# Performance work log

Measured on AMD Instinct MI355X. Metric: run time of the kernel, lower is better.

## Reference

```python
import jax, jax.numpy as jnp
import numpy as np

B, T, C, H = 2, 2048, 1024, 16
HD = C // H  # head dim = 64


def setup_inputs() -> dict:
    key = jax.random.key(0)
    ks = jax.random.split(key, 5)
    s = 1.0 / np.sqrt(C)
    return {
        "x": jax.random.normal(ks[0], (B, T, C), dtype=jnp.float32),
        "W_attn": jax.random.normal(ks[1], (3 * C, C), dtype=jnp.float32) * s,
        "b_attn": jax.random.normal(ks[2], (3 * C,), dtype=jnp.float32) * 0.02,
        "W_proj": jax.random.normal(ks[3], (C, C), dtype=jnp.float32) * s,
        "b_proj": jax.random.normal(ks[4], (C,), dtype=jnp.float32) * 0.02,
    }


def reference(x, W_attn, b_attn, W_proj, b_proj):
    Bx, Tx, Cx = x.shape
    # fused QKV projection (torch Linear: x @ W.T + b)
    qkv = x @ W_attn.T + b_attn                      # [B,T,3C]
    q, k, v = jnp.split(qkv, 3, axis=-1)
    # [B,T,C] -> [B,H,T,hd]
    q = q.reshape(Bx, Tx, H, HD).transpose(0, 2, 1, 3)
    k = k.reshape(Bx, Tx, H, HD).transpose(0, 2, 1, 3)
    v = v.reshape(Bx, Tx, H, HD).transpose(0, 2, 1, 3)
    scale = 1.0 / np.sqrt(HD)
    att = jnp.einsum('bhqd,bhkd->bhqk', q, k) * scale  # [B,H,T,T]
    causal = jnp.tril(jnp.ones((Tx, Tx), dtype=bool))
    att = jnp.where(causal[None, None], att, -jnp.inf)
    att = jax.nn.softmax(att, axis=-1)
    y = jnp.einsum('bhqk,bhkd->bhqd', att, v)          # [B,H,T,hd]
    y = y.transpose(0, 2, 1, 3).reshape(Bx, Tx, Cx)
    return y @ W_proj.T + b_proj
```

## Files before the change

### kernel.cpp

```cpp
#include <hip/hip_runtime.h>

typedef unsigned short ushort_t;
typedef __bf16 bf16x8 __attribute__((ext_vector_type(8)));
typedef float f32x4 __attribute__((ext_vector_type(4)));
typedef unsigned u32x4 __attribute__((ext_vector_type(4)));

__device__ inline ushort_t f2bf(float f) {
  unsigned int u = __builtin_bit_cast(unsigned int, f);
  u += 0x7fff + ((u >> 16) & 1);
  return (ushort_t)(u >> 16);
}

__device__ inline unsigned pk_bf(float a, float b) {
  unsigned r;
  asm("v_cvt_pk_bf16_f32 %0, %1, %2" : "=v"(r) : "v"(a), "v"(b));
  return r;
}

__device__ inline void async_ld16(const ushort_t* g, const ushort_t* l) {
  __builtin_amdgcn_global_load_lds(
      (const __attribute__((address_space(1))) void*)g,
      (__attribute__((address_space(3))) void*)l, 16, 0, 0);
}

template <int IMM>
__device__ inline void waitcnt_barrier() {
  asm volatile("" ::: "memory");
  __builtin_amdgcn_s_waitcnt(IMM);
  __builtin_amdgcn_s_barrier();
  asm volatile("" ::: "memory");
}

__global__ void cvt_all(const float* __restrict__ x, const float* __restrict__ wa,
                        const float* __restrict__ wp, ushort_t* __restrict__ xb,
                        ushort_t* __restrict__ wab, ushort_t* __restrict__ wpb) {
  int i = blockIdx.x * 256 + threadIdx.x;
  const float* src;
  ushort_t* dst;
  int off;
  if (i < 1048576) { src = x; dst = xb; off = i; }
  else if (i < 1835008) { src = wa; dst = wab; off = i - 1048576; }
  else { src = wp; dst = wpb; off = i - 1835008; }
  float4 f = ((const float4*)src)[off];
  unsigned long long p = (unsigned long long)f2bf(f.x)
      | ((unsigned long long)f2bf(f.y) << 16)
      | ((unsigned long long)f2bf(f.z) << 32)
      | ((unsigned long long)f2bf(f.w) << 48);
  ((unsigned long long*)dst)[off] = p;
}

template <int BM, int BN, int IM, int JN, int MODE, int TPB>
__global__ __launch_bounds__(TPB) void gemm_bt(
    const ushort_t* __restrict__ A, const ushort_t* __restrict__ B,
    const float* __restrict__ bias, float* __restrict__ Cf,
    ushort_t* __restrict__ Cb, ushort_t* __restrict__ vtb,
    int M, int N, int K, int ldc, float qscale) {
  constexpr int NWN = BN / (JN * 16);
  constexpr int NL = (BM + BN) * 32 / (TPB * 8);
  constexpr int WIMM = 0x0F70 | NL;
  __shared__ __align__(16) ushort_t As[3][BM * 32];
  __shared__ __align__(16) ushort_t Bs[3][BN * 32];
  const int tid = threadIdx.x;
  const int wave = tid >> 6, lane = tid & 63;
  const int quad = lane >> 4, l16 = lane & 15;
  const int wr = wave / NWN, wc = wave % NWN;
  const int wm = wr * IM * 16, wn = wc * JN * 16;
  const int m0 = blockIdx.y * BM, n0 = blockIdx.x * BN;
  const ushort_t* Ag = A + (size_t)m0 * K;
  const ushort_t* Bg = B + (size_t)n0 * K;
  const int slot = (quad ^ ((l16 >> 1) & 3)) * 8;
  f32x4 acc[IM][JN] = {};

  auto stage = [&](int kt, int bsel) {
    int k0 = kt * 32;
#pragma unroll
    for (int p = 0; p < BM * 4 / TPB; ++p) {
      int ci = p * TPB + tid;
      int row = ci >> 2, ch = (ci & 3) ^ ((ci >> 3) & 3);
      async_ld16(Ag + (size_t)row * K + k0 + ch * 8, As[bsel] + (p * TPB + wave * 64) * 8);
    }
#pragma unroll
    for (int p = 0; p < BN * 4 / TPB; ++p) {
      int ci = p * TPB + tid;
      int row = ci >> 2, ch = (ci & 3) ^ ((ci >> 3) & 3);
      async_ld16(Bg + (size_t)row * K + k0 + ch * 8, Bs[bsel] + (p * TPB + wave * 64) * 8);
    }
  };

  const int KT = K / 32;
  stage(0, 0);
  stage(1, 1);
  for (int kt = 0; kt < KT; ++kt) {
    waitcnt_barrier<WIMM>();
    if (kt + 2 < KT) stage(kt + 2, (kt + 2) % 3);
    const ushort_t* Ac = As[kt % 3];
    const ushort_t* Bc = Bs[kt % 3];
    bf16x8 af[IM], bfr[JN];
#pragma unroll
    for (int i = 0; i < IM; ++i)
      af[i] = *(const bf16x8*)(Ac + (wm + i * 16 + l16) * 32 + slot);
#pragma unroll
    for (int j = 0; j < JN; ++j)
      bfr[j] = *(const bf16x8*)(Bc + (wn + j * 16 + l16) * 32 + slot);
#pragma unroll
    for (int i = 0; i < IM; ++i)
#pragma unroll
      for (int j = 0; j < JN; ++j)
        acc[i][j] = __builtin_amdgcn_mfma_f32_16x16x32_bf16(af[i], bfr[j], acc[i][j], 0, 0, 0);
  }

  if (MODE == 1 && n0 >= 2048) {
#pragma unroll
    for (int j = 0; j < JN; ++j) {
      int col = n0 + wn + j * 16 + l16;
      int cv = col - 2048;
      float bv = bias[col];
      size_t rowbase = ((size_t)(cv >> 6)) * 64 + (cv & 63);
#pragma unroll
      for (int i = 0; i < IM; ++i) {
        int rowb = m0 + wm + i * 16 + quad * 4;
        int bb = rowb >> 11, t = rowb & 2047;
        uint2 pp;
        pp.x = pk_bf(acc[i][j][0] + bv, acc[i][j][1] + bv);
        pp.y = pk_bf(acc[i][j][2] + bv, acc[i][j][3] + bv);
        *(uint2*)(vtb + (((size_t)bb * 1024 + rowbase) * 2048 + t)) = pp;
      }
    }
    return;
  }
#pragma unroll
  for (int j = 0; j < JN; ++j) {
    int col = n0 + wn + j * 16 + l16;
    float bv = bias[col];
    float sc = (MODE == 1 && col < 1024) ? qscale : 1.0f;
#pragma unroll
    for (int i = 0; i < IM; ++i)
#pragma unroll
      for (int r = 0; r < 4; ++r) {
        int row = m0 + wm + i * 16 + quad * 4 + r;
        float v = (acc[i][j][r] + bv) * sc;
        if (MODE == 1)
          Cb[(size_t)row * ldc + col] = f2bf(v);
        else
          Cf[(size_t)row * ldc + col] = v;
      }
  }
}

__global__ __launch_bounds__(512, 4) void flash9(
    const ushort_t* __restrict__ qk, const ushort_t* __restrict__ vt,
    ushort_t* __restrict__ y) {
  __shared__ __align__(16) ushort_t Kb[2][2][4096];
  __shared__ __align__(16) ushort_t Vb[2][2][4096];
  const int tid = threadIdx.x, wave = tid >> 6, lane = tid & 63;
  const int quad = lane >> 4, l16 = lane & 15;
  const int r7 = l16 & 7;
  const int fK = (l16 & 3) | (((l16 >> 2) & 1) << 2);
  const int kbase = (16 * (l16 >> 2) + (l16 & 3)) * 64;
  const int xx = blockIdx.x, bh = blockIdx.y;
  const int Q = (bh < 16) ? (15 - xx) : xx;
  const int b = bh >> 4, h = bh & 15;
  const int bT = b * 2048;
  const int qw = Q * 128 + wave * 16;

  bf16x8 qf[2];
  {
    const ushort_t* qrow = qk + (size_t)(bT + qw + l16) * 2048 + h * 64 + quad * 8;
    qf[0] = *(const bf16x8*)(qrow);
    qf[1] = *(const bf16x8*)(qrow + 32);
  }

  auto stage1 = [&](int kt, int bsel, int u) {
    int k0 = kt * 64;
    int row = tid >> 3;
    int chk = (tid & 7) ^ ((row & 3) | (((row >> 4) & 1) << 2));
    int chv = (tid & 7) ^ (row & 7);
    async_ld16(qk + (size_t)(bT + k0 + row) * 2048 + 1024 + h * 64 + chk * 8,
               Kb[bsel][u] + wave * 512);
    async_ld16(vt + (size_t)(bh * 64 + row) * 2048 + k0 + chv * 8,
               Vb[bsel][u] + wave * 512);
  };
  auto stageS = [&](int s, int bsel) { stage1(2 * s, bsel, 0); stage1(2 * s + 1, bsel, 1); };

  f32x4 o[4] = {};
  float lac0 = 0.f, lac1 = 0.f;
  const int NS = Q + 1;

  stageS(0, 0);
  for (int s = 0; s < NS; ++s) {
    const int cur = s & 1;
    waitcnt_barrier<0x0F70>();
    if (s + 1 < NS) stageS(s + 1, cur ^ 1);
    __builtin_amdgcn_s_setprio(1);
    bf16x8 pf[2][2];
#pragma unroll
    for (int u = 0; u < 2; ++u) {
      const ushort_t* Kc = Kb[cur][u];
      const ushort_t* Vc = Vb[cur][u];
      bf16x8 kf[4][2];
#pragma unroll
      for (int j = 0; j < 4; ++j)
#pragma unroll
        for (int ks = 0; ks < 2; ++ks)
          kf[j][ks] = *(const bf16x8*)(Kc + kbase + j * 256 + (((ks * 4 + quad) ^ fK) * 8));
      f32x4 sr[4] = {};
#pragma unroll
      for (int ks = 0; ks < 2; ++ks)
#pragma unroll
        for (int j = 0; j < 4; ++j)
          sr[j] = __builtin_amdgcn_mfma_f32_16x16x32_bf16(kf[j][ks], qf[ks], sr[j], 0, 0, 0);
      if (s == NS - 1) {
        int qloc = qw + l16;
        int kt0 = (2 * s + u) * 64;
#pragma unroll
        for (int j = 0; j < 4; ++j)
#pragma unroll
          for (int r = 0; r < 4; ++r)
            if (kt0 + quad * 16 + j * 4 + r > qloc) sr[j][r] = -1e30f;
      }
#pragma unroll
      for (int j = 0; j < 4; ++j)
#pragma unroll
        for (int r = 0; r < 4; ++r)
          sr[j][r] = exp2f(sr[j][r]);
#pragma unroll
      for (int ks = 0; ks < 2; ++ks) {
        u32x4 w;
        w[0] = pk_bf(sr[2 * ks][0], sr[2 * ks][1]);
        w[1] = pk_bf(sr[2 * ks][2], sr[2 * ks][3]);
        w[2] = pk_bf(sr[2 * ks + 1][0], sr[2 * ks + 1][1]);
        w[3] = pk_bf(sr[2 * ks + 1][2], sr[2 * ks + 1][3]);
        pf[u][ks] = __builtin_bit_cast(bf16x8, w);
      }
#pragma unroll
      for (int j = 0; j < 4; ++j)
#pragma unroll
        for (int r = 0; r < 4; ++r) {
          if (j & 1) lac1 += sr[j][r]; else lac0 += sr[j][r];
        }
#pragma unroll
      for (int ks = 0; ks < 2; ++ks)
#pragma unroll
        for (int j = 0; j < 4; ++j) {
          bf16x8 vf = *(const bf16x8*)(Vc + (j * 16 + l16) * 64 + (((ks + 2 * quad) ^ r7) * 8));
          o[j] = __builtin_amdgcn_mfma_f32_16x16x32_bf16(vf, pf[u][ks], o[j], 0, 0, 0);
        }
    }
    __builtin_amdgcn_s_setprio(0);
  }

  {
    float l = lac0 + lac1;
    l += __shfl_xor(l, 16, 64);
    l += __shfl_xor(l, 32, 64);
    float inv = 1.f / l;
    size_t row = (size_t)(bT + qw + l16);
#pragma unroll
    for (int j = 0; j < 4; ++j) {
      uint2 pp;
      pp.x = pk_bf(o[j][0] * inv, o[j][1] * inv);
      pp.y = pk_bf(o[j][2] * inv, o[j][3] * inv);
      *(uint2*)(y + row * 1024 + h * 64 + j * 16 + quad * 4) = pp;
    }
  }
}

extern "C" void kernel_launch(void* const* d_in, const int* in_sizes, int n_in,
                              void* d_out, int out_size, void* d_ws, size_t ws_size,
                              hipStream_t stream) {
  const float* x  = (const float*)d_in[0];
  const float* Wa = (const float*)d_in[1];
  const float* ba = (const float*)d_in[2];
  const float* Wp = (const float*)d_in[3];
  const float* bp = (const float*)d_in[4];
  float* out = (float*)d_out;
  char* ws = (char*)d_ws;
  ushort_t* xb  = (ushort_t*)(ws);
  ushort_t* Wab = (ushort_t*)(ws + 8388608);
  ushort_t* Wpb = (ushort_t*)(ws + 14680064);
  ushort_t* qkb = (ushort_t*)(ws + 16777216);
  ushort_t* yb  = (ushort_t*)(ws + 33554432);
  ushort_t* vtb = (ushort_t*)(ws + 41943040);

  cvt_all<<<8192, 256, 0, stream>>>(x, Wa, Wp, xb, Wab, Wpb);
  gemm_bt<128, 128, 4, 2, 1, 512><<<dim3(24, 32), 512, 0, stream>>>(
      xb, Wab, ba, nullptr, qkb, vtb, 4096, 3072, 1024, 2048, 0.18033688011112042f);
  flash9<<<dim3(16, 32), 512, 0, stream>>>(qkb, vtb, yb);
  gemm_bt<64, 64, 2, 2, 0, 256><<<dim3(16, 64), 256, 0, stream>>>(
      yb, Wpb, bp, out, nullptr, nullptr, 4096, 1024, 1024, 1024, 1.0f);
}
```

Before: 178.4 us.

## Split long causal query tiles across two blocks with atomic-counter partial merge

Work in the flash attention kernel is rebalanced so that every block processes about the same number of key tiles. The long causal rows (query tiles 8-15) are split at key tile 17 between two blocks, and odd blocks also take a short query tile. The partial unnormalised outputs and row sums go to a float workspace, and an atomic counter per tile lets the second finisher combine both halves and write the result. The counters are reset in the conversion kernel. Occupancy hint drops from 4 to 2 blocks per CU, and the change adds extra global traffic and fences for the partials.

```diff
diff --git a/kernel.cpp b/kernel.cpp
--- a/kernel.cpp
+++ b/kernel.cpp
@@ -33,7 +33,9 @@
 
 __global__ void cvt_all(const float* __restrict__ x, const float* __restrict__ wa,
                         const float* __restrict__ wp, ushort_t* __restrict__ xb,
-                        ushort_t* __restrict__ wab, ushort_t* __restrict__ wpb) {
+                        ushort_t* __restrict__ wab, ushort_t* __restrict__ wpb,
+                        int* __restrict__ cnt) {
+  if (blockIdx.x == 0) cnt[threadIdx.x] = 0;
   int i = blockIdx.x * 256 + threadIdx.x;
   const float* src;
   ushort_t* dst;
@@ -147,31 +149,25 @@
   }
 }
 
-__global__ __launch_bounds__(512, 4) void flash9(
+__global__ __launch_bounds__(512, 2) void flash10(
     const ushort_t* __restrict__ qk, const ushort_t* __restrict__ vt,
-    ushort_t* __restrict__ y) {
+    ushort_t* __restrict__ y, float* __restrict__ pO, float* __restrict__ pl,
+    int* __restrict__ cnt) {
   __shared__ __align__(16) ushort_t Kb[2][2][4096];
   __shared__ __align__(16) ushort_t Vb[2][2][4096];
+  __shared__ int sflag;
   const int tid = threadIdx.x, wave = tid >> 6, lane = tid & 63;
   const int quad = lane >> 4, l16 = lane & 15;
   const int r7 = l16 & 7;
   const int fK = (l16 & 3) | (((l16 >> 2) & 1) << 2);
   const int kbase = (16 * (l16 >> 2) + (l16 & 3)) * 64;
-  const int xx = blockIdx.x, bh = blockIdx.y;
-  const int Q = (bh < 16) ? (15 - xx) : xx;
+  const int w = blockIdx.x, bh = blockIdx.y;
   const int b = bh >> 4, h = bh & 15;
   const int bT = b * 2048;
-  const int qw = Q * 128 + wave * 16;
-
-  bf16x8 qf[2];
-  {
-    const ushort_t* qrow = qk + (size_t)(bT + qw + l16) * 2048 + h * 64 + quad * 8;
-    qf[0] = *(const bf16x8*)(qrow);
-    qf[1] = *(const bf16x8*)(qrow + 32);
-  }
-
-  auto stage1 = [&](int kt, int bsel, int u) {
-    int k0 = kt * 64;
+  const int nseg = (w & 1) ? 2 : 1;
+
+  auto stage1 = [&](int t, int bsel, int u) {
+    int k0 = t * 64;
     int row = tid >> 3;
     int chk = (tid & 7) ^ ((row & 3) | (((row >> 4) & 1) << 2));
     int chv = (tid & 7) ^ (row & 7);
@@ -180,87 +176,142 @@
     async_ld16(vt + (size_t)(bh * 64 + row) * 2048 + k0 + chv * 8,
                Vb[bsel][u] + wave * 512);
   };
-  auto stageS = [&](int s, int bsel) { stage1(2 * s, bsel, 0); stage1(2 * s + 1, bsel, 1); };
-
-  f32x4 o[4] = {};
-  float lac0 = 0.f, lac1 = 0.f;
-  const int NS = Q + 1;
-
-  stageS(0, 0);
-  for (int s = 0; s < NS; ++s) {
-    const int cur = s & 1;
-    waitcnt_barrier<0x0F70>();
-    if (s + 1 < NS) stageS(s + 1, cur ^ 1);
-    __builtin_amdgcn_s_setprio(1);
-    bf16x8 pf[2][2];
-#pragma unroll
-    for (int u = 0; u < 2; ++u) {
-      const ushort_t* Kc = Kb[cur][u];
-      const ushort_t* Vc = Vb[cur][u];
-      bf16x8 kf[4][2];
-#pragma unroll
-      for (int j = 0; j < 4; ++j)
+
+  for (int seg = 0; seg < nseg; ++seg) {
+    int j, tbeg, tend, isfin;
+    if (w & 1) {
+      if (seg == 0) { j = 15 - (w >> 1); tbeg = 17; tend = 2 * j + 2; isfin = 0; }
+      else          { j = w >> 1;        tbeg = 0;  tend = 2 * j + 2; isfin = 1; }
+    } else          { j = 15 - (w >> 1); tbeg = 0;  tend = 17;        isfin = 0; }
+    const int qt0 = j * 128;
+    const int qw = qt0 + wave * 16;
+    const int qloc = qw + l16;
+
+    bf16x8 qf[2];
+    {
+      const ushort_t* qrow = qk + (size_t)(bT + qloc) * 2048 + h * 64 + quad * 8;
+      qf[0] = *(const bf16x8*)(qrow);
+      qf[1] = *(const bf16x8*)(qrow + 32);
+    }
+
+    auto stageS = [&](int s, int bsel) {
+      int t0 = tbeg + 2 * s;
+      stage1(t0, bsel, 0);
+      if (t0 + 1 < tend) stage1(t0 + 1, bsel, 1);
+    };
+
+    f32x4 o[4] = {};
+    float lac0 = 0.f, lac1 = 0.f;
+    const int NSs = (tend - tbeg + 1) >> 1;
+
+    stageS(0, 0);
+    for (int s = 0; s < NSs; ++s) {
+      const int cur = s & 1;
+      waitcnt_barrier<0x0F70>();
+      if (s + 1 < NSs) stageS(s + 1, cur ^ 1);
+      __builtin_amdgcn_s_setprio(1);
+      const int t0 = tbeg + 2 * s;
+#pragma unroll
+      for (int u = 0; u < 2; ++u) {
+        if (u == 1 && t0 + 1 >= tend) break;
+        const int kt = t0 + u;
+        const ushort_t* Kc = Kb[cur][u];
+        const ushort_t* Vc = Vb[cur][u];
+        bf16x8 kf[4][2];
+#pragma unroll
+        for (int jj = 0; jj < 4; ++jj)
+#pragma unroll
+          for (int ks = 0; ks < 2; ++ks)
+            kf[jj][ks] = *(const bf16x8*)(Kc + kbase + jj * 256 + (((ks * 4 + quad) ^ fK) * 8));
+        f32x4 sr[4] = {};
 #pragma unroll
         for (int ks = 0; ks < 2; ++ks)
-          kf[j][ks] = *(const bf16x8*)(Kc + kbase + j * 256 + (((ks * 4 + quad) ^ fK) * 8));
-      f32x4 sr[4] = {};
-#pragma unroll
-      for (int ks = 0; ks < 2; ++ks)
-#pragma unroll
-        for (int j = 0; j < 4; ++j)
-          sr[j] = __builtin_amdgcn_mfma_f32_16x16x32_bf16(kf[j][ks], qf[ks], sr[j], 0, 0, 0);
-      if (s == NS - 1) {
-        int qloc = qw + l16;
-        int kt0 = (2 * s + u) * 64;
-#pragma unroll
-        for (int j = 0; j < 4; ++j)
+#pragma unroll
+          for (int jj = 0; jj < 4; ++jj)
+            sr[jj] = __builtin_amdgcn_mfma_f32_16x16x32_bf16(kf[jj][ks], qf[ks], sr[jj], 0, 0, 0);
+        if (kt >= 2 * j) {
+#pragma unroll
+          for (int jj = 0; jj < 4; ++jj)
+#pragma unroll
+            for (int r = 0; r < 4; ++r)
+              if (kt * 64 + quad * 16 + jj * 4 + r > qloc) sr[jj][r] = -1e30f;
+        }
+#pragma unroll
+        for (int jj = 0; jj < 4; ++jj)
 #pragma unroll
           for (int r = 0; r < 4; ++r)
-            if (kt0 + quad * 16 + j * 4 + r > qloc) sr[j][r] = -1e30f;
-      }
-#pragma unroll
-      for (int j = 0; j < 4; ++j)
-#pragma unroll
-        for (int r = 0; r < 4; ++r)
-          sr[j][r] = exp2f(sr[j][r]);
-#pragma unroll
-      for (int ks = 0; ks < 2; ++ks) {
-        u32x4 w;
-        w[0] = pk_bf(sr[2 * ks][0], sr[2 * ks][1]);
-        w[1] = pk_bf(sr[2 * ks][2], sr[2 * ks][3]);
-        w[2] = pk_bf(sr[2 * ks + 1][0], sr[2 * ks + 1][1]);
-        w[3] = pk_bf(sr[2 * ks + 1][2], sr[2 * ks + 1][3]);
-        pf[u][ks] = __builtin_bit_cast(bf16x8, w);
-      }
-#pragma unroll
-      for (int j = 0; j < 4; ++j)
-#pragma unroll
-        for (int r = 0; r < 4; ++r) {
-          if (j & 1) lac1 += sr[j][r]; else lac0 += sr[j][r];
+            sr[jj][r] = exp2f(sr[jj][r]);
+        bf16x8 pf[2];
+#pragma unroll
+        for (int ks = 0; ks < 2; ++ks) {
+          u32x4 wd;
+          wd[0] = pk_bf(sr[2 * ks][0], sr[2 * ks][1]);
+          wd[1] = pk_bf(sr[2 * ks][2], sr[2 * ks][3]);
+          wd[2] = pk_bf(sr[2 * ks + 1][0], sr[2 * ks + 1][1]);
+          wd[3] = pk_bf(sr[2 * ks + 1][2], sr[2 * ks + 1][3]);
+          pf[ks] = __builtin_bit_cast(bf16x8, wd);
         }
 #pragma unroll
-      for (int ks = 0; ks < 2; ++ks)
-#pragma unroll
-        for (int j = 0; j < 4; ++j) {
-          bf16x8 vf = *(const bf16x8*)(Vc + (j * 16 + l16) * 64 + (((ks + 2 * quad) ^ r7) * 8));
-          o[j] = __builtin_amdgcn_mfma_f32_16x16x32_bf16(vf, pf[u][ks], o[j], 0, 0, 0);
-        }
-    }
-    __builtin_amdgcn_s_setprio(0);
-  }
-
-  {
+        for (int jj = 0; jj < 4; ++jj)
+#pragma unroll
+          for (int r = 0; r < 4; ++r) {
+            if (jj & 1) lac1 += sr[jj][r]; else lac0 += sr[jj][r];
+          }
+#pragma unroll
+        for (int ks = 0; ks < 2; ++ks)
+#pragma unroll
+          for (int jj = 0; jj < 4; ++jj) {
+            bf16x8 vf = *(const bf16x8*)(Vc + (jj * 16 + l16) * 64 + (((ks + 2 * quad) ^ r7) * 8));
+            o[jj] = __builtin_amdgcn_mfma_f32_16x16x32_bf16(vf, pf[ks], o[jj], 0, 0, 0);
+          }
+      }
+      __builtin_amdgcn_s_setprio(0);
+    }
+
     float l = lac0 + lac1;
     l += __shfl_xor(l, 16, 64);
     l += __shfl_xor(l, 32, 64);
-    float inv = 1.f / l;
-    size_t row = (size_t)(bT + qw + l16);
-#pragma unroll
-    for (int j = 0; j < 4; ++j) {
-      uint2 pp;
-      pp.x = pk_bf(o[j][0] * inv, o[j][1] * inv);
-      pp.y = pk_bf(o[j][2] * inv, o[j][3] * inv);
-      *(uint2*)(y + row * 1024 + h * 64 + j * 16 + quad * 4) = pp;
+    const int rowloc = wave * 16 + l16;
+
+    if (isfin) {
+      float inv = 1.f / l;
+      size_t row = (size_t)(bT + qt0 + rowloc);
+#pragma unroll
+      for (int jj = 0; jj < 4; ++jj) {
+        uint2 pp;
+        pp.x = pk_bf(o[jj][0] * inv, o[jj][1] * inv);
+        pp.y = pk_bf(o[jj][2] * inv, o[jj][3] * inv);
+        *(uint2*)(y + row * 1024 + h * 64 + jj * 16 + quad * 4) = pp;
+      }
+    } else {
+      const int tile = bh * 8 + (j - 8);
+      const int slot = w & 1;
+      float* po = pO + ((size_t)(tile * 2 + slot)) * 8192;
+#pragma unroll
+      for (int jj = 0; jj < 4; ++jj)
+        *(f32x4*)(po + rowloc * 64 + jj * 16 + quad * 4) = o[jj];
+      if (quad == 0) pl[(tile * 2 + slot) * 128 + rowloc] = l;
+      __syncthreads();
+      if (tid == 0) {
+        __threadfence();
+        sflag = atomicAdd(&cnt[tile], 1);
+      }
+      __syncthreads();
+      if (sflag == 1) {
+        __threadfence();
+        const float* qo = pO + ((size_t)(tile * 2 + (slot ^ 1))) * 8192;
+        float lo = pl[(tile * 2 + (slot ^ 1)) * 128 + rowloc];
+        float inv = 1.f / (l + lo);
+        size_t row = (size_t)(bT + qt0 + rowloc);
+#pragma unroll
+        for (int jj = 0; jj < 4; ++jj) {
+          f32x4 q4 = *(const f32x4*)(qo + rowloc * 64 + jj * 16 + quad * 4);
+          uint2 pp;
+          pp.x = pk_bf((o[jj][0] + q4[0]) * inv, (o[jj][1] + q4[1]) * inv);
+          pp.y = pk_bf((o[jj][2] + q4[2]) * inv, (o[jj][3] + q4[3]) * inv);
+          *(uint2*)(y + row * 1024 + h * 64 + jj * 16 + quad * 4) = pp;
+        }
+      }
     }
   }
 }
@@ -281,11 +332,14 @@
   ushort_t* qkb = (ushort_t*)(ws + 16777216);
   ushort_t* yb  = (ushort_t*)(ws + 33554432);
   ushort_t* vtb = (ushort_t*)(ws + 41943040);
-
-  cvt_all<<<8192, 256, 0, stream>>>(x, Wa, Wp, xb, Wab, Wpb);
+  float*    pO  = (float*)(ws + 67108864);
+  float*    pl  = (float*)(ws + 83886080);
+  int*      cnt = (int*)(ws + 84934656);
+
+  cvt_all<<<8192, 256, 0, stream>>>(x, Wa, Wp, xb, Wab, Wpb, cnt);
   gemm_bt<128, 128, 4, 2, 1, 512><<<dim3(24, 32), 512, 0, stream>>>(
       xb, Wab, ba, nullptr, qkb, vtb, 4096, 3072, 1024, 2048, 0.18033688011112042f);
-  flash9<<<dim3(16, 32), 512, 0, stream>>>(qkb, vtb, yb);
+  flash10<<<dim3(16, 32), 512, 0, stream>>>(qkb, vtb, yb, pO, pl, cnt);
   gemm_bt<64, 64, 2, 2, 0, 256><<<dim3(16, 64), 256, 0, stream>>>(
       yb, Wpb, bp, out, nullptr, nullptr, 4096, 1024, 1024, 1024, 1.0f);
 }
```

Result: slower. 285.8 us (+60.2%).
